# Kernel tuning notes

Measured on AMD Instinct MI355X. Metric: run time of the kernel, lower is better.

## Reference

```python
import jax, jax.numpy as jnp
import numpy as np

S, L, K = 4, 256, 32          # num_states, seq length, neighbors
ORIG_H, EMB_H, EXV, RANK = 128, 256, 384, 16


def _integrate(x, Wq, Wk, seq_idx, emb_idx, hidden, rank):
    """AttentionIntegrator.forward: QK^T softmax -> double mean -> softmax -> weighted pool of raw x."""
    x = jnp.moveaxis(x, (seq_idx, emb_idx), (-2, -1))
    orig_shape = x.shape
    Ls = orig_shape[-2]
    xf = x.reshape(-1, Ls, hidden)               # (B, Ls, hidden)
    B = xf.shape[0]
    q = (xf @ Wq.T).reshape(B, Ls, rank, hidden)  # head_dim == hidden
    k = (xf @ Wk.T).reshape(B, Ls, rank, hidden)
    scale = 1.0 / jnp.sqrt(jnp.asarray(hidden, xf.dtype))
    scores = jnp.einsum('blhd,bmhd->bhlm', q, k) * scale
    attn = jax.nn.softmax(scores, axis=-1)        # (B, rank, Ls, Ls)
    w = jax.nn.softmax(attn.mean(axis=(1, 2)), axis=-1)  # (B, Ls)
    pooled = jnp.einsum('bl,bld->bd', w, xf)      # (B, hidden)
    return (pooled.reshape(*orig_shape[:-2], hidden),
            w.reshape(*orig_shape[:-2], Ls))


def setup_inputs() -> dict:
    key = jax.random.key(0)
    ks = jax.random.split(key, 12)
    sc = lambda fan_in: 1.0 / np.sqrt(fan_in)
    return {
        'h_V':    jax.random.normal(ks[0], (S, L, ORIG_H), jnp.float32),
        'h_EXV':  jax.random.normal(ks[1], (S, L, K, EXV), jnp.float32),
        'W_hV':   jax.random.normal(ks[2], (EMB_H, ORIG_H), jnp.float32) * sc(ORIG_H),
        'b_hV':   jnp.zeros((EMB_H,), jnp.float32),
        'Wq_hv':  jax.random.normal(ks[3], (RANK * EMB_H, EMB_H), jnp.float32) * sc(EMB_H),
        'Wk_hv':  jax.random.normal(ks[4], (RANK * EMB_H, EMB_H), jnp.float32) * sc(EMB_H),
        'Wq_ce':  jax.random.normal(ks[5], (RANK * EXV, EXV), jnp.float32) * sc(EXV),
        'Wk_ce':  jax.random.normal(ks[6], (RANK * EXV, EXV), jnp.float32) * sc(EXV),
        'W_ce':   jax.random.normal(ks[7], (EMB_H, EXV), jnp.float32) * sc(EXV),
        'b_ce':   jnp.zeros((EMB_H,), jnp.float32),
        'Wq_sce': jax.random.normal(ks[8], (RANK * EMB_H, EMB_H), jnp.float32) * sc(EMB_H),
        'Wk_sce': jax.random.normal(ks[9], (RANK * EMB_H, EMB_H), jnp.float32) * sc(EMB_H),
    }


def reference(h_V, h_EXV, W_hV, b_hV, Wq_hv, Wk_hv, Wq_ce, Wk_ce, W_ce, b_ce, Wq_sce, Wk_sce):
    # diffmodel.get_weights
    hv = h_V @ W_hV.T + b_hV                                  # (S, L, EMB_H)
    h_V_int, h_V_w = _integrate(hv, Wq_hv, Wk_hv, 0, 2, EMB_H, RANK)   # pool over states
    # chemical environment: pool over k neighbors per (state, position)
    ce, _local_w = _integrate(h_EXV, Wq_ce, Wk_ce, 2, 3, EXV, RANK)    # (S, L, EXV)
    ce = ce @ W_ce.T + b_ce                                   # (S, L, EMB_H)
    ce_int, ce_w = _integrate(ce, Wq_sce, Wk_sce, 0, 2, EMB_H, RANK)   # pool over states
    return (h_V_int[None], h_V_w[None], ce_int[None], ce_w[None])
```

## Files before the change

### kernel.cpp

```cpp
#include <hip/hip_runtime.h>

typedef _Float16 f16;
typedef _Float16 f16x8 __attribute__((ext_vector_type(8)));
typedef _Float16 f16x4 __attribute__((ext_vector_type(4)));
typedef float f32x4 __attribute__((ext_vector_type(4)));

#define MFMA16(a, b, c) __builtin_amdgcn_mfma_f32_16x16x32_f16(a, b, c, 0, 0, 0)
#define MFMA16K16(a, b, c) __builtin_amdgcn_mfma_f32_16x16x16f16(a, b, c, 0, 0, 0)

__global__ __launch_bounds__(256) void k_front(const float* __restrict__ Wq_hv,
                                               const float* __restrict__ Wk_hv,
                                               f16* __restrict__ mt_hv,
                                               const float* __restrict__ Wq_ce,
                                               const float* __restrict__ Wk_ce,
                                               f16* __restrict__ mt_ce,
                                               const float* __restrict__ Wq_sce,
                                               const float* __restrict__ Wk_sce,
                                               f16* __restrict__ mt_sce,
                                               const float* __restrict__ h_V,
                                               const float* __restrict__ W_hV,
                                               const float* __restrict__ b_hV,
                                               float* __restrict__ hv) {
    extern __shared__ __align__(16) char smem[];
    const int bid = blockIdx.x;
    const int t = threadIdx.x;

    if (bid < 1088) {
        const int h = bid & 15;
        const int y = bid >> 4;
        const float *Wq, *Wk;
        f16* MT;
        int H, ty;
        if (y < 16)      { Wq = Wq_hv;  Wk = Wk_hv;  MT = mt_hv;  H = 256; ty = y; }
        else if (y < 52) { Wq = Wq_ce;  Wk = Wk_ce;  MT = mt_ce;  H = 384; ty = y - 16; }
        else             { Wq = Wq_sce; Wk = Wk_sce; MT = mt_sce; H = 256; ty = y - 52; }

        const int ntile = H >> 6;
        const int nkk = H >> 5;
        const int frow = (ty / ntile) * 64;
        const int ecol = (ty % ntile) * 64;
        const int lane = t & 63;
        const int w = t >> 6;
        const int wr = w >> 1, wc = w & 1;

        f16(*As)[40] = (f16(*)[40])smem;
        f16(*Ks)[40] = (f16(*)[40])(smem + 5120);

        f32x4 acc[2][2] = {};
        const int d = t >> 3;
        const int e8 = (t & 7) * 8;

        for (int kk = 0; kk < nkk; ++kk) {
            const float* gq = Wq + (size_t)(h * H + kk * 32 + d) * H + ecol + e8;
            const float* gk = Wk + (size_t)(h * H + kk * 32 + d) * H + frow + e8;
            float q[8], k[8];
#pragma unroll
            for (int i = 0; i < 8; ++i) { q[i] = gq[i]; k[i] = gk[i]; }
            __syncthreads();
#pragma unroll
            for (int i = 0; i < 8; ++i) { As[e8 + i][d] = (f16)q[i]; Ks[e8 + i][d] = (f16)k[i]; }
            __syncthreads();
            f16x8 a[2], b[2];
#pragma unroll
            for (int rt = 0; rt < 2; ++rt)
                a[rt] = *(const f16x8*)&Ks[wr * 32 + rt * 16 + (lane & 15)][(lane >> 4) * 8];
#pragma unroll
            for (int nt = 0; nt < 2; ++nt)
                b[nt] = *(const f16x8*)&As[wc * 32 + nt * 16 + (lane & 15)][(lane >> 4) * 8];
#pragma unroll
            for (int rt = 0; rt < 2; ++rt)
#pragma unroll
                for (int nt = 0; nt < 2; ++nt)
                    acc[rt][nt] = MFMA16(a[rt], b[nt], acc[rt][nt]);
        }
#pragma unroll
        for (int rt = 0; rt < 2; ++rt)
#pragma unroll
            for (int nt = 0; nt < 2; ++nt)
#pragma unroll
                for (int j = 0; j < 4; ++j) {
                    int f = frow + wr * 32 + rt * 16 + (lane >> 4) * 4 + j;
                    int e = ecol + wc * 32 + nt * 16 + (lane & 15);
                    MT[(((size_t)h * nkk + (e >> 5)) * H + f) * 32 + (e & 31)] = (f16)acc[rt][nt][j];
                }
    } else {
        const int r0 = (bid - 1088) * 4;
        const int K = 128;
        float(*ins)[384] = (float(*)[384])smem;
        float(*Ws)[33] = (float(*)[33])(smem + 6144);
#pragma unroll
        for (int r = 0; r < 4; ++r)
            for (int off = t; off < K; off += 256)
                ins[r][off] = h_V[(size_t)(r0 + r) * K + off];
        float acc[4] = {};
        for (int d0 = 0; d0 < K; d0 += 32) {
            __syncthreads();
            for (int i = t; i < 256 * 32; i += 256) {
                int j = i >> 5, dd = i & 31;
                Ws[j][dd] = W_hV[(size_t)j * K + d0 + dd];
            }
            __syncthreads();
#pragma unroll 8
            for (int dd = 0; dd < 32; ++dd) {
                float wv = Ws[t][dd];
#pragma unroll
                for (int r = 0; r < 4; ++r) acc[r] += wv * ins[r][d0 + dd];
            }
        }
        float bv = b_hV[t];
#pragma unroll
        for (int r = 0; r < 4; ++r) hv[(size_t)(r0 + r) * 256 + t] = acc[r] + bv;
    }
}

__global__ __launch_bounds__(256) void k_lin(const float* __restrict__ in,
                                             const float* __restrict__ W,
                                             const float* __restrict__ bias,
                                             float* __restrict__ out, int K) {
    const int t = threadIdx.x;
    const int r0 = blockIdx.x * 4;
    __shared__ float ins[4][384];
    __shared__ float Ws[256][33];
#pragma unroll
    for (int r = 0; r < 4; ++r)
        for (int off = t; off < K; off += 256)
            ins[r][off] = in[(size_t)(r0 + r) * K + off];
    float acc[4] = {};
    for (int d0 = 0; d0 < K; d0 += 32) {
        __syncthreads();
        for (int i = t; i < 256 * 32; i += 256) {
            int j = i >> 5, dd = i & 31;
            Ws[j][dd] = W[(size_t)j * K + d0 + dd];
        }
        __syncthreads();
#pragma unroll 8
        for (int dd = 0; dd < 32; ++dd) {
            float wv = Ws[t][dd];
#pragma unroll
            for (int r = 0; r < 4; ++r) acc[r] += wv * ins[r][d0 + dd];
        }
    }
    float bv = bias[t];
#pragma unroll
    for (int r = 0; r < 4; ++r) out[(size_t)(r0 + r) * 256 + t] = acc[r] + bv;
}

__global__ __launch_bounds__(256) void k_small_int(const float* __restrict__ X,
                                                   const f16* __restrict__ MT,
                                                   float* __restrict__ wpart) {
    const int t = threadIdx.x;
    const int lane = t & 63;
    const int w = t >> 6;
    const int g = lane >> 4;
    const int l15 = lane & 15;
    const int pos0 = blockIdx.x * 8;
    const int h = blockIdx.y;

    __shared__ __align__(16) f16 Xs[32][264];
    __shared__ __align__(16) f16 Ts[32][264];

    {
        int row = t >> 3, d0 = (t & 7) * 32;
        int s = row & 3, p = row >> 2;
        const float* gx = X + (size_t)(s * 256 + pos0 + p) * 256 + d0;
#pragma unroll
        for (int i = 0; i < 32; i += 8) {
            float4 v0 = *(const float4*)(gx + i);
            float4 v1 = *(const float4*)(gx + i + 4);
            f16x8 o;
            o[0] = (f16)v0.x; o[1] = (f16)v0.y; o[2] = (f16)v0.z; o[3] = (f16)v0.w;
            o[4] = (f16)v1.x; o[5] = (f16)v1.y; o[6] = (f16)v1.z; o[7] = (f16)v1.w;
            *(f16x8*)&Xs[row][d0 + i] = o;
        }
    }
    __syncthreads();

    const f16* mh = MT + (size_t)h * 8 * 256 * 32;
    const int fb = w * 64 + l15;
    f32x4 acc[2][4] = {};
    f16x8 bq[4], bn[4];
#pragma unroll
    for (int nt = 0; nt < 4; ++nt)
        bq[nt] = *(const f16x8*)(mh + (size_t)(fb + nt * 16) * 32 + g * 8);
#pragma unroll
    for (int kk = 0; kk < 8; ++kk) {
        if (kk < 7) {
#pragma unroll
            for (int nt = 0; nt < 4; ++nt)
                bn[nt] = *(const f16x8*)(mh + ((size_t)(kk + 1) * 256 + fb + nt * 16) * 32 + g * 8);
        }
        f16x8 a[2];
#pragma unroll
        for (int mt = 0; mt < 2; ++mt)
            a[mt] = *(const f16x8*)&Xs[mt * 16 + l15][kk * 32 + g * 8];
#pragma unroll
        for (int mt = 0; mt < 2; ++mt)
#pragma unroll
            for (int nt = 0; nt < 4; ++nt)
                acc[mt][nt] = MFMA16(a[mt], bq[nt], acc[mt][nt]);
#pragma unroll
        for (int nt = 0; nt < 4; ++nt) bq[nt] = bn[nt];
    }
#pragma unroll
    for (int mt = 0; mt < 2; ++mt)
#pragma unroll
        for (int nt = 0; nt < 4; ++nt)
#pragma unroll
            for (int j = 0; j < 4; ++j)
                Ts[mt * 16 + g * 4 + j][w * 64 + nt * 16 + l15] = (f16)acc[mt][nt][j];
    __syncthreads();

    if (w < 2) {
        f32x4 sacc = {};
#pragma unroll
        for (int ks = 0; ks < 8; ++ks) {
            f16x8 a = *(const f16x8*)&Ts[w * 16 + l15][ks * 32 + g * 8];
            f16x8 b = *(const f16x8*)&Xs[w * 16 + l15][ks * 32 + g * 8];
            sacc = MFMA16(a, b, sacc);
        }
        if ((l15 >> 2) == g) {
            const float scale = 1.0f / 16.0f;
            float add = 0.f;
#pragma unroll
            for (int j = 0; j < 4; ++j) {
                float v = sacc[j] * scale;
                float m = v;
                m = fmaxf(m, __shfl_xor(m, 1));
                m = fmaxf(m, __shfl_xor(m, 2));
                float e = expf(v - m);
                float s2 = e;
                s2 += __shfl_xor(s2, 1);
                s2 += __shfl_xor(s2, 2);
                add += e / s2;
            }
            int pg = pos0 + w * 4 + g;
            wpart[((size_t)h * 256 + pg) * 4 + (l15 & 3)] = add;
        }
    }
}

__global__ __launch_bounds__(256) void k_small_fin(const float* __restrict__ wpart,
                                                   const float* __restrict__ X,
                                                   float* __restrict__ out_int,
                                                   float* __restrict__ out_w) {
    const int pos = blockIdx.x, t = threadIdx.x;
    __shared__ float red[64];
    __shared__ float ws[4];
    if (t < 64) red[t] = wpart[((size_t)(t >> 2) * 256 + pos) * 4 + (t & 3)];
    __syncthreads();
    if (t == 0) {
        float v[4];
#pragma unroll
        for (int s = 0; s < 4; ++s) {
            float x = 0.f;
            for (int hh = 0; hh < 16; ++hh) x += red[hh * 4 + s];
            v[s] = x * (1.0f / 64.0f);
        }
        float m = fmaxf(fmaxf(v[0], v[1]), fmaxf(v[2], v[3]));
        float sum = 0.f;
#pragma unroll
        for (int s = 0; s < 4; ++s) { v[s] = expf(v[s] - m); sum += v[s]; }
#pragma unroll
        for (int s = 0; s < 4; ++s) ws[s] = v[s] / sum;
    }
    __syncthreads();
    if (t < 4) out_w[pos * 4 + t] = ws[t];
    float v = 0.f;
#pragma unroll
    for (int s = 0; s < 4; ++s) v += ws[s] * X[(size_t)(s * 256 + pos) * 256 + t];
    out_int[(size_t)pos * 256 + t] = v;
}

__global__ __launch_bounds__(512) void k_mid(const float* __restrict__ Xg32,
                                             const f16* __restrict__ MTce,
                                             float* __restrict__ acc_out,
                                             const float* __restrict__ hv,
                                             const f16* __restrict__ MThv,
                                             float* __restrict__ wpart) {
    extern __shared__ __align__(16) char smem[];
    const int t = threadIdx.x;
    const int lane = t & 63;
    const int w = t >> 6;
    const int g = lane >> 4;
    const int l15 = lane & 15;

    if (blockIdx.x < 512) {
        const int bg = blockIdx.x;
        {
            const float* xg = Xg32 + (size_t)bg * 64 * 384;
#pragma unroll
            for (int p = 0; p < 6; ++p) {
                int idx = p * 512 + t;
                int row = idx / 48, s = idx - row * 48;
                int c = s ^ (row & 7);
                const float* src = xg + row * 384 + c * 8;
                float4 v0 = *(const float4*)src;
                float4 v1 = *(const float4*)(src + 4);
                f16x8 o;
                o[0] = (f16)v0.x; o[1] = (f16)v0.y; o[2] = (f16)v0.z; o[3] = (f16)v0.w;
                o[4] = (f16)v1.x; o[5] = (f16)v1.y; o[6] = (f16)v1.z; o[7] = (f16)v1.w;
                *(f16x8*)(smem + idx * 16) = o;
            }
        }
        __syncthreads();

        const float scale = 0.051031036307982884f;

        for (int h2 = 0; h2 < 2; ++h2) {
            const int h = h2 * 8 + w;
            const f16* mh = MTce + (size_t)h * 12 * 12288;

            f32x4 S2[2][2][2] = {};
            f16x8 A[2][2];
#pragma unroll
            for (int ft = 0; ft < 2; ++ft)
                A[0][ft] = *(const f16x8*)(mh + (size_t)(ft * 16 + l15) * 32 + g * 8);

            for (int c = 0; c < 12; ++c) {
                f32x4 acc[2][4] = {};
#pragma unroll
                for (int kk = 0; kk < 12; ++kk) {
                    const int step = c * 12 + kk;
                    {
                        int ns = step + 1;
                        int nc = ns / 12, nk = ns - nc * 12;
                        if (nc > 11) { nc = 11; nk = 11; }
#pragma unroll
                        for (int ft = 0; ft < 2; ++ft)
                            A[(step + 1) & 1][ft] =
                                *(const f16x8*)(mh + (size_t)nk * 12288 +
                                                (size_t)(nc * 32 + ft * 16 + l15) * 32 + g * 8);
                    }
                    f16x8 xb[4];
#pragma unroll
                    for (int mt = 0; mt < 4; ++mt) {
                        int row = mt * 16 + l15;
                        int ch = kk * 4 + g;
                        xb[mt] = *(const f16x8*)(smem + row * 768 + ((ch ^ (row & 7)) << 4));
                    }
                    __builtin_amdgcn_s_setprio(1);
#pragma unroll
                    for (int ft = 0; ft < 2; ++ft)
#pragma unroll
                        for (int mt = 0; mt < 4; ++mt)
                            acc[ft][mt] = MFMA16(A[step & 1][ft], xb[mt], acc[ft][mt]);
                    __builtin_amdgcn_s_setprio(0);
                }

                f16x4 bf[2][4];
#pragma unroll
                for (int ft = 0; ft < 2; ++ft)
#pragma unroll
                    for (int mt = 0; mt < 4; ++mt) {
                        f32x4 v = acc[ft][mt];
                        f16x4 o;
                        o[0] = (f16)v[0]; o[1] = (f16)v[1]; o[2] = (f16)v[2]; o[3] = (f16)v[3];
                        bf[ft][mt] = o;
                    }

#pragma unroll
                for (int b = 0; b < 2; ++b)
#pragma unroll
                    for (int ks = 0; ks < 2; ++ks)
#pragma unroll
                        for (int it = 0; it < 2; ++it) {
                            int row = b * 32 + it * 16 + l15;
                            int ch = c * 4 + ks * 2 + (g >> 1);
                            f16x4 av = *(const f16x4*)(smem + row * 768 +
                                                       ((ch ^ (row & 7)) << 4) + 8 * (g & 1));
#pragma unroll
                            for (int lt = 0; lt < 2; ++lt)
                                S2[b][it][lt] = MFMA16K16(av, bf[ks][2 * b + lt], S2[b][it][lt]);
                        }
            }

#pragma unroll
            for (int b = 0; b < 2; ++b)
#pragma unroll
                for (int it = 0; it < 2; ++it) {
                    f32x4 sum0 = S2[b][it][0];
                    f32x4 sum1 = S2[b][it][1];
                    float cs0 = 0.f, cs1 = 0.f;
#pragma unroll
                    for (int j = 0; j < 4; ++j) {
                        float v0 = sum0[j] * scale, v1 = sum1[j] * scale;
                        float m = fmaxf(v0, v1);
                        m = fmaxf(m, __shfl_xor(m, 1));
                        m = fmaxf(m, __shfl_xor(m, 2));
                        m = fmaxf(m, __shfl_xor(m, 4));
                        m = fmaxf(m, __shfl_xor(m, 8));
                        float e0 = __expf(v0 - m), e1 = __expf(v1 - m);
                        float s = e0 + e1;
                        s += __shfl_xor(s, 1);
                        s += __shfl_xor(s, 2);
                        s += __shfl_xor(s, 4);
                        s += __shfl_xor(s, 8);
                        float inv = 1.f / s;
                        cs0 += e0 * inv;
                        cs1 += e1 * inv;
                    }
                    cs0 += __shfl_xor(cs0, 16); cs0 += __shfl_xor(cs0, 32);
                    cs1 += __shfl_xor(cs1, 16); cs1 += __shfl_xor(cs1, 32);
                    if (lane < 16) {
                        float* o = acc_out + (((size_t)h * 1024 + bg * 2 + b) * 2 + it) * 32;
                        o[l15] = cs0;
                        o[16 + l15] = cs1;
                    }
                }
        }
    } else {
        const int bid2 = blockIdx.x - 512;
        const int pos0 = (bid2 & 31) * 8;
        const int h = bid2 >> 5;

        f16(*Xs)[264] = (f16(*)[264])smem;
        f16(*Ts)[264] = (f16(*)[264])(smem + 16896);

        if (t < 256) {
            int row = t >> 3, d0 = (t & 7) * 32;
            int s = row & 3, p = row >> 2;
            const float* gx = hv + (size_t)(s * 256 + pos0 + p) * 256 + d0;
#pragma unroll
            for (int i = 0; i < 32; i += 8) {
                float4 v0 = *(const float4*)(gx + i);
                float4 v1 = *(const float4*)(gx + i + 4);
                f16x8 o;
                o[0] = (f16)v0.x; o[1] = (f16)v0.y; o[2] = (f16)v0.z; o[3] = (f16)v0.w;
                o[4] = (f16)v1.x; o[5] = (f16)v1.y; o[6] = (f16)v1.z; o[7] = (f16)v1.w;
                *(f16x8*)&Xs[row][d0 + i] = o;
            }
        }
        __syncthreads();

        if (t < 256) {
            const f16* mh = MThv + (size_t)h * 8 * 256 * 32;
            const int fb = w * 64 + l15;
            f32x4 acc[2][4] = {};
            f16x8 bq[4], bn[4];
#pragma unroll
            for (int nt = 0; nt < 4; ++nt)
                bq[nt] = *(const f16x8*)(mh + (size_t)(fb + nt * 16) * 32 + g * 8);
#pragma unroll
            for (int kk = 0; kk < 8; ++kk) {
                if (kk < 7) {
#pragma unroll
                    for (int nt = 0; nt < 4; ++nt)
                        bn[nt] = *(const f16x8*)(mh + ((size_t)(kk + 1) * 256 + fb + nt * 16) * 32 + g * 8);
                }
                f16x8 a[2];
#pragma unroll
                for (int mt = 0; mt < 2; ++mt)
                    a[mt] = *(const f16x8*)&Xs[mt * 16 + l15][kk * 32 + g * 8];
#pragma unroll
                for (int mt = 0; mt < 2; ++mt)
#pragma unroll
                    for (int nt = 0; nt < 4; ++nt)
                        acc[mt][nt] = MFMA16(a[mt], bq[nt], acc[mt][nt]);
#pragma unroll
                for (int nt = 0; nt < 4; ++nt) bq[nt] = bn[nt];
            }
#pragma unroll
            for (int mt = 0; mt < 2; ++mt)
#pragma unroll
                for (int nt = 0; nt < 4; ++nt)
#pragma unroll
                    for (int j = 0; j < 4; ++j)
                        Ts[mt * 16 + g * 4 + j][w * 64 + nt * 16 + l15] = (f16)acc[mt][nt][j];
        }
        __syncthreads();

        if (t < 128) {
            f32x4 sacc = {};
#pragma unroll
            for (int ks = 0; ks < 8; ++ks) {
                f16x8 a = *(const f16x8*)&Ts[w * 16 + l15][ks * 32 + g * 8];
                f16x8 b = *(const f16x8*)&Xs[w * 16 + l15][ks * 32 + g * 8];
                sacc = MFMA16(a, b, sacc);
            }
            if ((l15 >> 2) == g) {
                const float scale = 1.0f / 16.0f;
                float add = 0.f;
#pragma unroll
                for (int j = 0; j < 4; ++j) {
                    float v = sacc[j] * scale;
                    float m = v;
                    m = fmaxf(m, __shfl_xor(m, 1));
                    m = fmaxf(m, __shfl_xor(m, 2));
                    float e = expf(v - m);
                    float s2 = e;
                    s2 += __shfl_xor(s2, 1);
                    s2 += __shfl_xor(s2, 2);
                    add += e / s2;
                }
                int pg = pos0 + w * 4 + g;
                wpart[((size_t)h * 256 + pg) * 4 + (l15 & 3)] = add;
            }
        }
    }
}

__global__ __launch_bounds__(256) void k_back(const float* __restrict__ accp,
                                              const float* __restrict__ exv,
                                              float* __restrict__ pooled,
                                              const float* __restrict__ wpart,
                                              const float* __restrict__ hv,
                                              float* __restrict__ out_int,
                                              float* __restrict__ out_w) {
    const int t = threadIdx.x;
    __shared__ float ww[32];
    __shared__ float red[64];
    __shared__ float ws[4];

    if (blockIdx.x < 1024) {
        const int b = blockIdx.x;
        if (t < 32) {
            float s = 0.f;
#pragma unroll
            for (int h = 0; h < 16; ++h) {
                s += accp[(((size_t)h * 1024 + b) * 2 + 0) * 32 + t];
                s += accp[(((size_t)h * 1024 + b) * 2 + 1) * 32 + t];
            }
            s *= (1.0f / 512.0f);
            float m = s;
            m = fmaxf(m, __shfl_xor(m, 1));
            m = fmaxf(m, __shfl_xor(m, 2));
            m = fmaxf(m, __shfl_xor(m, 4));
            m = fmaxf(m, __shfl_xor(m, 8));
            m = fmaxf(m, __shfl_xor(m, 16));
            float e = __expf(s - m);
            float sum = e;
            sum += __shfl_xor(sum, 1);
            sum += __shfl_xor(sum, 2);
            sum += __shfl_xor(sum, 4);
            sum += __shfl_xor(sum, 8);
            sum += __shfl_xor(sum, 16);
            ww[t] = e / sum;
        }
        __syncthreads();
        for (int d = t; d < 384; d += 256) {
            float v = 0.f;
#pragma unroll
            for (int m = 0; m < 32; ++m) v += ww[m] * exv[((size_t)b * 32 + m) * 384 + d];
            pooled[(size_t)b * 384 + d] = v;
        }
    } else {
        const int pos = blockIdx.x - 1024;
        if (t < 64) red[t] = wpart[((size_t)(t >> 2) * 256 + pos) * 4 + (t & 3)];
        __syncthreads();
        if (t == 0) {
            float v[4];
#pragma unroll
            for (int s = 0; s < 4; ++s) {
                float x = 0.f;
                for (int hh = 0; hh < 16; ++hh) x += red[hh * 4 + s];
                v[s] = x * (1.0f / 64.0f);
            }
            float m = fmaxf(fmaxf(v[0], v[1]), fmaxf(v[2], v[3]));
            float sum = 0.f;
#pragma unroll
            for (int s = 0; s < 4; ++s) { v[s] = expf(v[s] - m); sum += v[s]; }
#pragma unroll
            for (int s = 0; s < 4; ++s) ws[s] = v[s] / sum;
        }
        __syncthreads();
        if (t < 4) out_w[pos * 4 + t] = ws[t];
        float v = 0.f;
#pragma unroll
        for (int s = 0; s < 4; ++s) v += ws[s] * hv[(size_t)(s * 256 + pos) * 256 + t];
        out_int[(size_t)pos * 256 + t] = v;
    }
}

extern "C" void kernel_launch(void* const* d_in, const int* in_sizes, int n_in,
                              void* d_out, int out_size, void* d_ws, size_t ws_size,
                              hipStream_t stream) {
    const float* h_V    = (const float*)d_in[0];
    const float* h_EXV  = (const float*)d_in[1];
    const float* W_hV   = (const float*)d_in[2];
    const float* b_hV   = (const float*)d_in[3];
    const float* Wq_hv  = (const float*)d_in[4];
    const float* Wk_hv  = (const float*)d_in[5];
    const float* Wq_ce  = (const float*)d_in[6];
    const float* Wk_ce  = (const float*)d_in[7];
    const float* W_ce   = (const float*)d_in[8];
    const float* b_ce   = (const float*)d_in[9];
    const float* Wq_sce = (const float*)d_in[10];
    const float* Wk_sce = (const float*)d_in[11];
    float* out = (float*)d_out;

    char* ws = (char*)d_ws;
    f16*   mt_hv  = (f16*)(ws + 0);
    f16*   mt_sce = (f16*)(ws + 2097152);
    f16*   mt_ce  = (f16*)(ws + 4194304);
    float* hv     = (float*)(ws + 8912896);
    float* ce     = (float*)(ws + 9961472);
    float* accp   = (float*)(ws + 11010048);
    float* pooled = (float*)(ws + 15204352);
    float* wpart  = (float*)(ws + 16777216);

    k_front<<<1344, 256, 39936, stream>>>(Wq_hv, Wk_hv, mt_hv,
                                          Wq_ce, Wk_ce, mt_ce,
                                          Wq_sce, Wk_sce, mt_sce,
                                          h_V, W_hV, b_hV, hv);
    k_mid<<<1024, 512, 49152, stream>>>(h_EXV, mt_ce, accp, hv, mt_hv, wpart);
    k_back<<<1280, 256, 0, stream>>>(accp, h_EXV, pooled, wpart, hv,
                                     out + 0, out + 65536);
    k_lin<<<256, 256, 0, stream>>>(pooled, W_ce, b_ce, ce, 384);
    k_small_int<<<dim3(32, 16), 256, 0, stream>>>(ce, mt_sce, wpart);
    k_small_fin<<<256, 256, 0, stream>>>(wpart, ce, out + 66560, out + 132096);
}
```

Before: 286.8 us.

## Double-buffer weight tiles in k_front, deepen A-fragment prefetch in k_mid, use __expf

In the weight-product part of k_front, the shared-memory staging tiles become double-buffered. The next k-slice's global loads are issued before the MFMAs on the current slice, and one barrier per iteration replaces two. In k_mid, the A-fragment register prefetch moves from one step ahead to three steps ahead, using a 4-slot ring, to hide more global-load latency. The price is extra VGPRs, which could lower occupancy. Softmax exponentials switch from expf to the fast __expf intrinsic, giving up a little accuracy to save instructions.

```diff
diff --git a/kernel.cpp b/kernel.cpp
--- a/kernel.cpp
+++ b/kernel.cpp
@@ -43,35 +43,54 @@
         const int w = t >> 6;
         const int wr = w >> 1, wc = w & 1;
 
-        f16(*As)[40] = (f16(*)[40])smem;
-        f16(*Ks)[40] = (f16(*)[40])(smem + 5120);
+        f16(*As)[64][40] = (f16(*)[64][40])smem;
+        f16(*Ks)[64][40] = (f16(*)[64][40])(smem + 10240);
 
         f32x4 acc[2][2] = {};
         const int d = t >> 3;
         const int e8 = (t & 7) * 8;
 
+        {
+            const float* gq = Wq + (size_t)(h * H + d) * H + ecol + e8;
+            const float* gk = Wk + (size_t)(h * H + d) * H + frow + e8;
+#pragma unroll
+            for (int i = 0; i < 8; ++i) {
+                As[0][e8 + i][d] = (f16)gq[i];
+                Ks[0][e8 + i][d] = (f16)gk[i];
+            }
+        }
+        __syncthreads();
+
         for (int kk = 0; kk < nkk; ++kk) {
-            const float* gq = Wq + (size_t)(h * H + kk * 32 + d) * H + ecol + e8;
-            const float* gk = Wk + (size_t)(h * H + kk * 32 + d) * H + frow + e8;
             float q[8], k[8];
-#pragma unroll
-            for (int i = 0; i < 8; ++i) { q[i] = gq[i]; k[i] = gk[i]; }
-            __syncthreads();
-#pragma unroll
-            for (int i = 0; i < 8; ++i) { As[e8 + i][d] = (f16)q[i]; Ks[e8 + i][d] = (f16)k[i]; }
-            __syncthreads();
+            if (kk + 1 < nkk) {
+                const float* gq = Wq + (size_t)(h * H + (kk + 1) * 32 + d) * H + ecol + e8;
+                const float* gk = Wk + (size_t)(h * H + (kk + 1) * 32 + d) * H + frow + e8;
+#pragma unroll
+                for (int i = 0; i < 8; ++i) { q[i] = gq[i]; k[i] = gk[i]; }
+            }
+            const int cur = kk & 1;
             f16x8 a[2], b[2];
 #pragma unroll
             for (int rt = 0; rt < 2; ++rt)
-                a[rt] = *(const f16x8*)&Ks[wr * 32 + rt * 16 + (lane & 15)][(lane >> 4) * 8];
+                a[rt] = *(const f16x8*)&Ks[cur][wr * 32 + rt * 16 + (lane & 15)][(lane >> 4) * 8];
 #pragma unroll
             for (int nt = 0; nt < 2; ++nt)
-                b[nt] = *(const f16x8*)&As[wc * 32 + nt * 16 + (lane & 15)][(lane >> 4) * 8];
+                b[nt] = *(const f16x8*)&As[cur][wc * 32 + nt * 16 + (lane & 15)][(lane >> 4) * 8];
 #pragma unroll
             for (int rt = 0; rt < 2; ++rt)
 #pragma unroll
                 for (int nt = 0; nt < 2; ++nt)
                     acc[rt][nt] = MFMA16(a[rt], b[nt], acc[rt][nt]);
+            if (kk + 1 < nkk) {
+                const int nxt = (kk + 1) & 1;
+#pragma unroll
+                for (int i = 0; i < 8; ++i) {
+                    As[nxt][e8 + i][d] = (f16)q[i];
+                    Ks[nxt][e8 + i][d] = (f16)k[i];
+                }
+                __syncthreads();
+            }
         }
 #pragma unroll
         for (int rt = 0; rt < 2; ++rt)
@@ -227,7 +246,7 @@
                 float m = v;
                 m = fmaxf(m, __shfl_xor(m, 1));
                 m = fmaxf(m, __shfl_xor(m, 2));
-                float e = expf(v - m);
+                float e = __expf(v - m);
                 float s2 = e;
                 s2 += __shfl_xor(s2, 1);
                 s2 += __shfl_xor(s2, 2);
@@ -259,7 +278,7 @@
         float m = fmaxf(fmaxf(v[0], v[1]), fmaxf(v[2], v[3]));
         float sum = 0.f;
 #pragma unroll
-        for (int s = 0; s < 4; ++s) { v[s] = expf(v[s] - m); sum += v[s]; }
+        for (int s = 0; s < 4; ++s) { v[s] = __expf(v[s] - m); sum += v[s]; }
 #pragma unroll
         for (int s = 0; s < 4; ++s) ws[s] = v[s] / sum;
     }
@@ -311,23 +330,27 @@
             const f16* mh = MTce + (size_t)h * 12 * 12288;
 
             f32x4 S2[2][2][2] = {};
-            f16x8 A[2][2];
-#pragma unroll
-            for (int ft = 0; ft < 2; ++ft)
-                A[0][ft] = *(const f16x8*)(mh + (size_t)(ft * 16 + l15) * 32 + g * 8);
+            f16x8 A[4][2];
+#pragma unroll
+            for (int s0 = 0; s0 < 3; ++s0) {
+                int nc = s0 / 12, nk = s0 % 12;
+#pragma unroll
+                for (int ft = 0; ft < 2; ++ft)
+                    A[s0 & 3][ft] = *(const f16x8*)(mh + (size_t)nk * 12288 +
+                                                    (size_t)(nc * 32 + ft * 16 + l15) * 32 + g * 8);
+            }
 
             for (int c = 0; c < 12; ++c) {
                 f32x4 acc[2][4] = {};
 #pragma unroll
                 for (int kk = 0; kk < 12; ++kk) {
-                    const int step = c * 12 + kk;
                     {
-                        int ns = step + 1;
-                        int nc = ns / 12, nk = ns - nc * 12;
+                        int nc = c + (kk + 3) / 12;
+                        int nk = (kk + 3) % 12;
                         if (nc > 11) { nc = 11; nk = 11; }
 #pragma unroll
                         for (int ft = 0; ft < 2; ++ft)
-                            A[(step + 1) & 1][ft] =
+                            A[(kk + 3) & 3][ft] =
                                 *(const f16x8*)(mh + (size_t)nk * 12288 +
                                                 (size_t)(nc * 32 + ft * 16 + l15) * 32 + g * 8);
                     }
@@ -343,7 +366,7 @@
                     for (int ft = 0; ft < 2; ++ft)
 #pragma unroll
                         for (int mt = 0; mt < 4; ++mt)
-                            acc[ft][mt] = MFMA16(A[step & 1][ft], xb[mt], acc[ft][mt]);
+                            acc[ft][mt] = MFMA16(A[kk & 3][ft], xb[mt], acc[ft][mt]);
                     __builtin_amdgcn_s_setprio(0);
                 }
 
@@ -486,7 +509,7 @@
                     float m = v;
                     m = fmaxf(m, __shfl_xor(m, 1));
                     m = fmaxf(m, __shfl_xor(m, 2));
-                    float e = expf(v - m);
+                    float e = __expf(v - m);
                     float s2 = e;
                     s2 += __shfl_xor(s2, 1);
                     s2 += __shfl_xor(s2, 2);
@@ -558,7 +581,7 @@
             float m = fmaxf(fmaxf(v[0], v[1]), fmaxf(v[2], v[3]));
             float sum = 0.f;
 #pragma unroll
-            for (int s = 0; s < 4; ++s) { v[s] = expf(v[s] - m); sum += v[s]; }
+            for (int s = 0; s < 4; ++s) { v[s] = __expf(v[s] - m); sum += v[s]; }
 #pragma unroll
             for (int s = 0; s < 4; ++s) ws[s] = v[s] / sum;
         }
```

After: 280.5 us, median of 2. -2.2%, faster.
